# Kernel optimization log

Hardware: AMD Instinct MI355X
Metric: run time of the kernel (lower is better)

Reference implementation:

```python
import jax, jax.numpy as jnp
import numpy as np

K_SIZE = 5  # kernel_size=[5]


def setup_inputs() -> dict:
    key = jax.random.key(0)
    k1, k2 = jax.random.split(key)
    bs, N, h, w, c = 4, 8, 256, 256, 1
    frames = jax.random.normal(k1, (bs, N, h, w, c), dtype=jnp.float32)
    core = jax.random.normal(k2, (bs, h, w, N * K_SIZE * K_SIZE * c), dtype=jnp.float32)
    return {"frames": frames, "core": core}


def _kpn_filter(frames, core):
    # frames: (bs, N, h, w, c); core: (bs, h, w, N*K*K*c)
    bs, N, h, w, c = frames.shape
    K = K_SIZE
    # _convert_dict: raw reshape of core to (bs, N, h, w, c, K*K)
    core_r = jnp.reshape(core, (bs, N, h, w, c, K * K))
    p = K // 2
    fpad = jnp.pad(frames, ((0, 0), (0, 0), (p, p), (p, p), (0, 0)))
    # K*K shifted views stacked on last axis: (bs, N, h, w, c, K*K)
    img_stack = jnp.stack(
        [fpad[:, :, i:i + h, j:j + w, :] for i in range(K) for j in range(K)],
        axis=-1,
    )
    # per-pixel dynamic-kernel weighted sum
    pred_img_i = jnp.sum(core_r * img_stack, axis=-1)  # (bs, N, h, w, c)
    # single kernel size -> mean over kernel axis is identity
    pred_img = jnp.mean(pred_img_i, axis=1)  # (bs, h, w, c), mean over burst N
    return pred_img, pred_img_i


def reference(frames, core):
    return _kpn_filter(frames, core)
```

## Files before the change

### kernel.cpp

```cpp
#include <hip/hip_runtime.h>

#define H 256
#define W 256

typedef float f4 __attribute__((ext_vector_type(4)));

__global__ __launch_bounds__(256, 4)
void kpn_quad(const float* __restrict__ frames, const float* __restrict__ core,
              float* __restrict__ pred, float* __restrict__ pred_i) {
  __shared__ f4 smem[8 * 5 * 10];
  __shared__ f4 red[64];

  const int tid = threadIdx.x;
  const int bid = blockIdx.x;
  const int blk = (bid & 7) * 1024 + (bid >> 3);
  const int xq  = blk & 7;
  const int y   = (blk >> 3) & 255;
  const int b   = blk >> 11;

  const int n = tid >> 5;
  const int q = (tid >> 2) & 7;
  const int j = tid & 3;

  const int g = ((b * 8 + n) * 256 + y) * 64 + xq * 8 + q;
  const f4* c4 = (const f4*)(core + (size_t)g * 100);
  f4 wv[7];
#pragma unroll
  for (int m = 0; m < 6; ++m) {
    wv[m] = c4[4 * m + j];
  }
  wv[6] = c4[24];
  __builtin_amdgcn_sched_barrier(0);

  for (int i = tid; i < 400; i += 256) {
    const int nn  = i / 50;
    const int rem = i - nn * 50;
    const int r   = rem / 10;
    const int c   = rem - r * 10;
    const int yy  = y + r - 2;
    const int x4  = xq * 32 + (c - 1) * 4;
    f4 v = {0.f, 0.f, 0.f, 0.f};
    if ((unsigned)yy < (unsigned)H && (unsigned)x4 <= 252u) {
      v = *(const f4*)(frames + ((size_t)(b * 8 + nn) * H + yy) * W + x4);
    }
    smem[i] = v;
  }
#pragma unroll
  for (int m = 0; m < 7; ++m) {
    asm volatile("" : "+v"(wv[m]));
  }
  __syncthreads();

  f4 w4[5][3];
#pragma unroll
  for (int ki = 0; ki < 5; ++ki) {
    const f4* row = &smem[(n * 5 + ki) * 10 + q];
    w4[ki][0] = row[0]; w4[ki][1] = row[1]; w4[ki][2] = row[2];
  }

  f4 acc = {0.f, 0.f, 0.f, 0.f};
#define DO_F(J, M, E)                                                     \
  { constexpr int f  = 16 * (M) + 4 * (J) + (E);                          \
    constexpr int p  = f / 25, kd = f % 25;                               \
    constexpr int ki = kd / 5, kj = kd % 5, wx = p + kj + 2;              \
    acc[p] += wv[M][E] * w4[ki][wx >> 2][wx & 3]; }
#define DO4(J, M) DO_F(J, M, 0) DO_F(J, M, 1) DO_F(J, M, 2) DO_F(J, M, 3)
  switch (j) {
    case 0: DO4(0,0) DO4(0,1) DO4(0,2) DO4(0,3) DO4(0,4) DO4(0,5) DO4(0,6) break;
    case 1: DO4(1,0) DO4(1,1) DO4(1,2) DO4(1,3) DO4(1,4) DO4(1,5) break;
    case 2: DO4(2,0) DO4(2,1) DO4(2,2) DO4(2,3) DO4(2,4) DO4(2,5) break;
    default:DO4(3,0) DO4(3,1) DO4(3,2) DO4(3,3) DO4(3,4) DO4(3,5) break;
  }
#undef DO4
#undef DO_F

#pragma unroll
  for (int c = 0; c < 4; ++c) {
    acc[c] += __shfl_xor(acc[c], 1, 64);
    acc[c] += __shfl_xor(acc[c], 2, 64);
  }

  if (j == 0) red[tid >> 2] = acc;
  __syncthreads();
  if (tid < 32) {
    const int qq = tid >> 2, p = tid & 3;
    float s = 0.f;
#pragma unroll
    for (int k = 0; k < 8; ++k) {
      s += red[k * 8 + qq][p];
    }
    s *= 0.125f;
    __builtin_nontemporal_store(
        s, pred + ((size_t)b * 256 + y) * 256 + xq * 32 + tid);
  }

  float out = (j == 0) ? acc[0] : (j == 1) ? acc[1] : (j == 2) ? acc[2] : acc[3];
  __builtin_nontemporal_store(out, pred_i + (size_t)g * 4 + j);
}

extern "C" void kernel_launch(void* const* d_in, const int* in_sizes, int n_in,
                              void* d_out, int out_size, void* d_ws, size_t ws_size,
                              hipStream_t stream) {
  const float* frames = (const float*)d_in[0];
  const float* core   = (const float*)d_in[1];
  float* pred   = (float*)d_out;
  float* pred_i = pred + (size_t)4 * H * W;

  hipLaunchKernelGGL(kpn_quad, dim3(8192), dim3(256), 0, stream,
                     frames, core, pred, pred_i);
}
```

Before: 37.40 us.

## Process two output rows per block to share the frame halo tile

Each block now covers a pair of adjacent output rows with 512 threads instead of one row with 256. The shared-memory frame tile grows from 5 to 6 rows per frame, so the halo rows loaded from global memory are shared by both rows. This cuts redundant frame reads, about 400 versus 480 float4 per row pair, and halves the block count. The kernel is dominated by streaming the core tensor, so the frame traffic saved is small, and the larger blocks may change occupancy and scheduling.

```diff
diff --git a/kernel.cpp b/kernel.cpp
--- a/kernel.cpp
+++ b/kernel.cpp
@@ -5,23 +5,26 @@
 
 typedef float f4 __attribute__((ext_vector_type(4)));
 
-__global__ __launch_bounds__(256, 4)
-void kpn_quad(const float* __restrict__ frames, const float* __restrict__ core,
-              float* __restrict__ pred, float* __restrict__ pred_i) {
-  __shared__ f4 smem[8 * 5 * 10];
-  __shared__ f4 red[64];
+__global__ __launch_bounds__(512, 4)
+void kpn_ypair(const float* __restrict__ frames, const float* __restrict__ core,
+               float* __restrict__ pred, float* __restrict__ pred_i) {
+  __shared__ f4 smem[8 * 6 * 10];
+  __shared__ f4 red[128];
 
   const int tid = threadIdx.x;
   const int bid = blockIdx.x;
-  const int blk = (bid & 7) * 1024 + (bid >> 3);
+  const int blk = (bid & 7) * 512 + (bid >> 3);
   const int xq  = blk & 7;
-  const int y   = (blk >> 3) & 255;
-  const int b   = blk >> 11;
+  const int yp  = (blk >> 3) & 127;
+  const int b   = blk >> 10;
+  const int y0  = yp * 2;
 
-  const int n = tid >> 5;
-  const int q = (tid >> 2) & 7;
-  const int j = tid & 3;
+  const int n  = tid >> 6;
+  const int yl = (tid >> 5) & 1;
+  const int q  = (tid >> 2) & 7;
+  const int j  = tid & 3;
 
+  const int y = y0 + yl;
   const int g = ((b * 8 + n) * 256 + y) * 64 + xq * 8 + q;
   const f4* c4 = (const f4*)(core + (size_t)g * 100);
   f4 wv[7];
@@ -32,18 +35,18 @@
   wv[6] = c4[24];
   __builtin_amdgcn_sched_barrier(0);
 
-  for (int i = tid; i < 400; i += 256) {
-    const int nn  = i / 50;
-    const int rem = i - nn * 50;
+  if (tid < 480) {
+    const int nn  = tid / 60;
+    const int rem = tid - nn * 60;
     const int r   = rem / 10;
     const int c   = rem - r * 10;
-    const int yy  = y + r - 2;
+    const int yy  = y0 + r - 2;
     const int x4  = xq * 32 + (c - 1) * 4;
     f4 v = {0.f, 0.f, 0.f, 0.f};
     if ((unsigned)yy < (unsigned)H && (unsigned)x4 <= 252u) {
       v = *(const f4*)(frames + ((size_t)(b * 8 + nn) * H + yy) * W + x4);
     }
-    smem[i] = v;
+    smem[(nn * 6 + r) * 10 + c] = v;
   }
 #pragma unroll
   for (int m = 0; m < 7; ++m) {
@@ -54,7 +57,7 @@
   f4 w4[5][3];
 #pragma unroll
   for (int ki = 0; ki < 5; ++ki) {
-    const f4* row = &smem[(n * 5 + ki) * 10 + q];
+    const f4* row = &smem[(n * 6 + yl + ki) * 10 + q];
     w4[ki][0] = row[0]; w4[ki][1] = row[1]; w4[ki][2] = row[2];
   }
 
@@ -80,18 +83,20 @@
     acc[c] += __shfl_xor(acc[c], 2, 64);
   }
 
-  if (j == 0) red[tid >> 2] = acc;
+  if (j == 0) red[yl * 64 + n * 8 + q] = acc;
   __syncthreads();
-  if (tid < 32) {
-    const int qq = tid >> 2, p = tid & 3;
+  if (tid < 64) {
+    const int ylr = tid >> 5;
+    const int px  = tid & 31;
+    const int qq  = px >> 2, p = px & 3;
     float s = 0.f;
 #pragma unroll
     for (int k = 0; k < 8; ++k) {
-      s += red[k * 8 + qq][p];
+      s += red[ylr * 64 + k * 8 + qq][p];
     }
     s *= 0.125f;
     __builtin_nontemporal_store(
-        s, pred + ((size_t)b * 256 + y) * 256 + xq * 32 + tid);
+        s, pred + ((size_t)b * 256 + y0 + ylr) * 256 + xq * 32 + px);
   }
 
   float out = (j == 0) ? acc[0] : (j == 1) ? acc[1] : (j == 2) ? acc[2] : acc[3];
@@ -106,6 +111,6 @@
   float* pred   = (float*)d_out;
   float* pred_i = pred + (size_t)4 * H * W;
 
-  hipLaunchKernelGGL(kpn_quad, dim3(8192), dim3(256), 0, stream,
+  hipLaunchKernelGGL(kpn_ypair, dim3(4096), dim3(512), 0, stream,
                      frames, core, pred, pred_i);
 }
```

Measured after the change: 38.32 us. 1.02x slower.
